# Kernel optimization log

Hardware: AMD Instinct MI355X
Metric: run time of the kernel (lower is better)

Reference implementation:

```python
import jax, jax.numpy as jnp
import numpy as np

B, N, P, K = 4, 8192, 2048, 16
C_IN, C_OUT, DIMS = 64, 128, 3
C_MID = C_OUT // 4                      # 32 (C_in != 0 branch)
DM = min(int(np.ceil(C_OUT / C_IN)), 4) # 2, depth multiplier for SepConv
C_DENSE = C_OUT // 2                    # 64, dense-projected feature dim
C_CAT = C_MID + C_DENSE                 # 96, lifted + projected features


def setup_inputs() -> dict:
    key = jax.random.key(0)
    ks = jax.random.split(key, 12)
    g = lambda k, shape, fan: jax.random.normal(k, shape, jnp.float32) / np.sqrt(fan).astype(np.float32)
    return {
        "pts": jax.random.normal(ks[0], (B, N, DIMS), jnp.float32),
        "fts": jax.random.normal(ks[1], (B, N, C_IN), jnp.float32),
        # PointCNN.dense: Linear(C_in, C_out//2) + ELU
        "dense_W": g(ks[2], (C_IN, C_DENSE), C_IN), "dense_b": jnp.zeros((C_DENSE,), jnp.float32),
        # XConv.dense1/dense2: Linear(dims,C_mid)+ELU, Linear(C_mid,C_mid)+ELU
        "d1_W": g(ks[3], (DIMS, C_MID), DIMS), "d1_b": jnp.zeros((C_MID,), jnp.float32),
        "d2_W": g(ks[4], (C_MID, C_MID), C_MID), "d2_b": jnp.zeros((C_MID,), jnp.float32),
        # conv2d: Conv2d(dims, K*K, (1,K)) + ELU, weight (out, in, kW)
        "conv_W": g(ks[5], (K * K, DIMS, K), DIMS * K), "conv_b": jnp.zeros((K * K,), jnp.float32),
        # dep_conv1/2: depthwise Conv2d(K, K*K, (1,K), groups=K); weight (group, mult, kW)
        "dw1_W": g(ks[6], (K, K, K), K), "dw1_b": jnp.zeros((K, K), jnp.float32),
        "dw2_W": g(ks[7], (K, K, K), K), "dw2_b": jnp.zeros((K, K), jnp.float32),
        # end_conv SepConv: depthwise (C_CAT groups, DM mult, (1,K)) then pointwise 1x1 -> C_OUT, ELU
        "sep_dw_W": g(ks[8], (C_CAT, DM, K), K), "sep_dw_b": jnp.zeros((C_CAT, DM), jnp.float32),
        "sep_pw_W": g(ks[9], (C_OUT, C_CAT, DM), C_CAT * DM), "sep_pw_b": jnp.zeros((C_OUT,), jnp.float32),
    }


def _fps(pts, npoint):
    """Iterative farthest point sampling (deterministic start at index 0)."""
    b, n, _ = pts.shape
    dist0 = jnp.full((b, n), 1e10, pts.dtype)
    far0 = jnp.zeros((b,), jnp.int32)

    def step(carry, _):
        dist, far = carry
        centroid = jnp.take_along_axis(pts, far[:, None, None], axis=1)  # [B,1,3]
        d = jnp.sum((pts - centroid) ** 2, -1)                            # [B,N]
        dist = jnp.minimum(dist, d)
        return (dist, jnp.argmax(dist, -1).astype(jnp.int32)), far

    _, idx = jax.lax.scan(step, (dist0, far0), None, length=npoint)  # [P,B]
    idx = idx.T                                                       # [B,P]
    return jnp.take_along_axis(pts, idx[..., None], axis=1)          # [B,P,3]


def reference(pts, fts, dense_W, dense_b, d1_W, d1_b, d2_W, d2_b,
              conv_W, conv_b, dw1_W, dw1_b, dw2_W, dw2_b,
              sep_dw_W, sep_dw_b, sep_pw_W, sep_pw_b):
    rep_pts = _fps(pts, P)                                            # [B,P,3]
    fts_d = jax.nn.elu(fts @ dense_W + dense_b)                       # [B,N,64]
    # KNN: squared distances rep->all points, K smallest
    d2 = (jnp.sum(rep_pts ** 2, -1)[..., None]
          - 2.0 * jnp.einsum('npc,nqc->npq', rep_pts, pts)
          + jnp.sum(pts ** 2, -1)[:, None, :])                        # [B,P,N]
    _, idx = jax.lax.top_k(-d2, K)                                    # [B,P,K]
    bidx = jnp.arange(B)[:, None, None]
    pts_reg = pts[bidx, idx]                                          # [B,P,K,3]
    fts_reg = fts_d[bidx, idx]                                        # [B,P,K,64]
    # XConv
    pl = pts_reg - rep_pts[:, :, None, :]                             # local coords
    lift = jax.nn.elu(jax.nn.elu(pl @ d1_W + d1_b) @ d2_W + d2_b)     # [B,P,K,C_MID]
    fts_cat = jnp.concatenate([lift, fts_reg], -1)                    # [B,P,K,C_CAT]
    X = jax.nn.elu(jnp.einsum('npkc,ock->npo', pl, conv_W) + conv_b).reshape(B, P, K, K)
    # depthwise convs over neighbor axis (spatial dim collapses to 1 -> einsum)
    X = jax.nn.elu(jnp.einsum('npij,jmi->npjm', X, dw1_W) + dw1_b)
    X = jnp.einsum('npij,jmi->npjm', X, dw2_W) + dw2_b
    fts_X = jnp.einsum('npab,npbc->npac', X, fts_cat)                 # [B,P,K,C_CAT]
    # separable end conv: depthwise over K, pointwise to C_OUT, ELU
    d = jnp.einsum('npkc,cmk->npcm', fts_X, sep_dw_W) + sep_dw_b
    fts_p = jax.nn.elu(jnp.einsum('npcm,ocm->npo', d, sep_pw_W) + sep_pw_b)  # [B,P,C_OUT]
    return rep_pts, fts_p
```

## Files before the change

### kernel.cpp

```cpp
#include <hip/hip_runtime.h>

#define BB 4
#define NN 8192
#define PP 2048
#define KNB 16
#define CIN 64
#define COUT 128

__device__ __forceinline__ float elu(float x) { return x > 0.0f ? x : expm1f(x); }

__device__ __forceinline__ unsigned fkey(float d) {
    unsigned u = __float_as_uint(d);
    unsigned m = (unsigned)((int)u >> 31);
    return u ^ (m | 0x80000000u);
}

__global__ __launch_bounds__(512) void fps_kernel(const float* __restrict__ pts,
                                                  float* __restrict__ rep) {
    const int b = blockIdx.x;
    const int t = threadIdx.x;
    const int lane = t & 63, wave = t >> 6;

    __shared__ float spx[NN];
    __shared__ float spy[NN];
    __shared__ float spz[NN];
    __shared__ unsigned long long partk[2][8];

    const float* pb = pts + (size_t)b * NN * 3;
    for (int i = t; i < NN; i += 512) {
        spx[i] = pb[3 * i + 0];
        spy[i] = pb[3 * i + 1];
        spz[i] = pb[3 * i + 2];
    }
    __syncthreads();

    float px[16], py[16], pz[16], dist[16];
#pragma unroll
    for (int r = 0; r < 16; ++r) {
        px[r] = spx[t * 16 + r];
        py[r] = spy[t * 16 + r];
        pz[r] = spz[t * 16 + r];
        dist[r] = 1e10f;
    }

    float cx = spx[0], cy = spy[0], cz = spz[0];
    if (t == 0) {
        rep[(size_t)b * PP * 3 + 0] = cx;
        rep[(size_t)b * PP * 3 + 1] = cy;
        rep[(size_t)b * PP * 3 + 2] = cz;
    }

    int buf = 0;
    for (int s = 1; s < PP; ++s) {
        float bv = -1.0f; int bi = 0;
#pragma unroll
        for (int r = 0; r < 16; ++r) {
            float dx = __fsub_rn(px[r], cx);
            float dy = __fsub_rn(py[r], cy);
            float dz = __fsub_rn(pz[r], cz);
            float d = __fadd_rn(__fadd_rn(__fmul_rn(dx, dx), __fmul_rn(dy, dy)), __fmul_rn(dz, dz));
            float nd = fminf(dist[r], d);
            dist[r] = nd;
            bool tk = nd > bv;
            bi = tk ? (t * 16 + r) : bi;
            bv = fmaxf(nd, bv);
        }
        unsigned long long k = ((unsigned long long)__float_as_uint(bv) << 32)
                             | (unsigned)(8191 - bi);
#pragma unroll
        for (int off = 32; off >= 1; off >>= 1) {
            unsigned long long o = __shfl_xor(k, off);
            k = o > k ? o : k;
        }
        if (lane == 0) partk[buf][wave] = k;
        __syncthreads();
        unsigned long long kk = partk[buf][0];
#pragma unroll
        for (int q = 1; q < 8; ++q) {
            unsigned long long c = partk[buf][q];
            kk = c > kk ? c : kk;
        }
        int widx = 8191 - (int)(unsigned)(kk & 0xFFFFFFFFULL);
        cx = spx[widx]; cy = spy[widx]; cz = spz[widx];
        if (t == 0) {
            float* rp = rep + ((size_t)b * PP + s) * 3;
            rp[0] = cx; rp[1] = cy; rp[2] = cz;
        }
        buf ^= 1;
    }
}

__global__ __launch_bounds__(256) void dense_kernel(const float* __restrict__ fts,
                                                    const float* __restrict__ W,
                                                    const float* __restrict__ bias,
                                                    float* __restrict__ out) {
    const int row = blockIdx.x * 4 + (threadIdx.x >> 6);
    const int c = threadIdx.x & 63;
    float v = fts[(size_t)row * 64 + c];
    float acc = bias[c];
#pragma unroll 8
    for (int k = 0; k < 64; ++k) acc = fmaf(__shfl(v, k), W[k * 64 + c], acc);
    out[(size_t)row * 64 + c] = elu(acc);
}

__global__ __launch_bounds__(256) void knn_kernel(const float* __restrict__ pts,
                                                  const float* __restrict__ rep,
                                                  int* __restrict__ kidx) {
    const int wid = blockIdx.x * 4 + (threadIdx.x >> 6);
    const int lane = threadIdx.x & 63;
    const int b = wid >> 11;
    const float* pb = pts + (size_t)b * NN * 3;

    float rx = rep[(size_t)wid * 3 + 0];
    float ry = rep[(size_t)wid * 3 + 1];
    float rz = rep[(size_t)wid * 3 + 2];
    float a = __fadd_rn(__fadd_rn(__fmul_rn(rx, rx), __fmul_rn(ry, ry)), __fmul_rn(rz, rz));

    unsigned long long key[16];
#pragma unroll
    for (int s = 0; s < 16; ++s) key[s] = ~0ULL;

    for (int j = lane; j < NN; j += 64) {
        float qx = pb[j * 3 + 0], qy = pb[j * 3 + 1], qz = pb[j * 3 + 2];
        float cc = __fadd_rn(__fadd_rn(__fmul_rn(qx, qx), __fmul_rn(qy, qy)), __fmul_rn(qz, qz));
        float bs = __fadd_rn(__fadd_rn(__fmul_rn(rx, qx), __fmul_rn(ry, qy)), __fmul_rn(rz, qz));
        float d2 = __fadd_rn(__fsub_rn(a, __fmul_rn(2.0f, bs)), cc);
        unsigned long long nk = ((unsigned long long)fkey(d2) << 32) | (unsigned)j;
        if (nk < key[15]) {
            key[15] = nk;
#pragma unroll
            for (int s2 = 15; s2 > 0; --s2) {
                unsigned long long u = key[s2 - 1], w = key[s2];
                bool sw = w < u;
                key[s2 - 1] = sw ? w : u;
                key[s2] = sw ? u : w;
            }
        }
    }

    int outv = 0;
#pragma unroll 1
    for (int r = 0; r < 16; ++r) {
        unsigned long long h = key[0];
#pragma unroll
        for (int off = 1; off < 64; off <<= 1) {
            unsigned long long o = __shfl_xor(h, off);
            h = (o < h) ? o : h;
        }
        if (lane == r) outv = (int)(unsigned)(h & 0xFFFFFFFFull);
        if (key[0] == h) {
#pragma unroll
            for (int s2 = 0; s2 < 15; ++s2) key[s2] = key[s2 + 1];
            key[15] = ~0ULL;
        }
    }
    if (lane < 16) kidx[(size_t)wid * 16 + lane] = outv;
}

__global__ __launch_bounds__(64) void xconv_kernel(
    const float* __restrict__ pts, const float* __restrict__ rep,
    const float* __restrict__ ftsd, const int* __restrict__ kidx,
    const float* __restrict__ d1W, const float* __restrict__ d1b,
    const float* __restrict__ d2W, const float* __restrict__ d2b,
    const float* __restrict__ convW, const float* __restrict__ convb,
    const float* __restrict__ dw1W, const float* __restrict__ dw1b,
    const float* __restrict__ dw2W, const float* __restrict__ dw2b,
    const float* __restrict__ sdwW, const float* __restrict__ sdwb,
    const float* __restrict__ spwW, const float* __restrict__ spwb,
    float* __restrict__ outp) {
    const int bp = blockIdx.x;
    const int b = bp >> 11;
    const int t = threadIdx.x;

    __shared__ float pl[16][3];
    __shared__ int nidx[16];
    __shared__ float fcat[16][96];
    __shared__ float A1[16][32];
    __shared__ float Xm[16][17];
    __shared__ float X2[16][17];
    __shared__ float X3[16][17];
    __shared__ float fX[16][97];
    __shared__ float dsep[192];

    if (t < 16) {
        int id = kidx[(size_t)bp * 16 + t];
        nidx[t] = id;
        const float* q = pts + ((size_t)b * NN + id) * 3;
        const float* rr = rep + (size_t)bp * 3;
        pl[t][0] = q[0] - rr[0];
        pl[t][1] = q[1] - rr[1];
        pl[t][2] = q[2] - rr[2];
    }
    __syncthreads();

#pragma unroll
    for (int k = 0; k < 16; ++k)
        fcat[k][32 + t] = ftsd[((size_t)b * NN + nidx[k]) * 64 + t];

#pragma unroll
    for (int r2 = 0; r2 < 8; ++r2) {
        int e = t + 64 * r2; int k = e >> 5, j = e & 31;
        float acc = d1b[j];
        acc = fmaf(pl[k][0], d1W[j], acc);
        acc = fmaf(pl[k][1], d1W[32 + j], acc);
        acc = fmaf(pl[k][2], d1W[64 + j], acc);
        A1[k][j] = elu(acc);
    }
    __syncthreads();

#pragma unroll
    for (int r2 = 0; r2 < 8; ++r2) {
        int e = t + 64 * r2; int k = e >> 5, j = e & 31;
        float acc = d2b[j];
#pragma unroll
        for (int c = 0; c < 32; ++c) acc = fmaf(A1[k][c], d2W[c * 32 + j], acc);
        fcat[k][j] = elu(acc);
    }
    __syncthreads();

#pragma unroll
    for (int r2 = 0; r2 < 4; ++r2) {
        int o = t + 64 * r2;
        float acc = convb[o];
#pragma unroll
        for (int c = 0; c < 3; ++c)
#pragma unroll
            for (int k = 0; k < 16; ++k)
                acc = fmaf(pl[k][c], convW[(o * 3 + c) * 16 + k], acc);
        Xm[o >> 4][o & 15] = elu(acc);
    }
    __syncthreads();

#pragma unroll
    for (int r2 = 0; r2 < 4; ++r2) {
        int e = t + 64 * r2; int j = e >> 4, m = e & 15;
        float acc = dw1b[e];
#pragma unroll
        for (int i = 0; i < 16; ++i) acc = fmaf(Xm[i][j], dw1W[e * 16 + i], acc);
        X2[j][m] = elu(acc);
    }
    __syncthreads();

#pragma unroll
    for (int r2 = 0; r2 < 4; ++r2) {
        int e = t + 64 * r2; int j = e >> 4, m = e & 15;
        float acc = dw2b[e];
#pragma unroll
        for (int i = 0; i < 16; ++i) acc = fmaf(X2[i][j], dw2W[e * 16 + i], acc);
        X3[j][m] = acc;
    }
    __syncthreads();

#pragma unroll
    for (int r2 = 0; r2 < 24; ++r2) {
        int e = t + 64 * r2; int a = e & 15, c = e >> 4;
        float acc = 0.0f;
#pragma unroll
        for (int q = 0; q < 16; ++q) acc = fmaf(X3[a][q], fcat[q][c], acc);
        fX[a][c] = acc;
    }
    __syncthreads();

#pragma unroll
    for (int r2 = 0; r2 < 3; ++r2) {
        int e = t + 64 * r2; int c = e >> 1;
        float acc = sdwb[e];
#pragma unroll
        for (int k = 0; k < 16; ++k) acc = fmaf(fX[k][c], sdwW[e * 16 + k], acc);
        dsep[e] = acc;
    }
    __syncthreads();

#pragma unroll
    for (int r2 = 0; r2 < 2; ++r2) {
        int o = t + 64 * r2;
        float acc = spwb[o];
#pragma unroll 16
        for (int e2 = 0; e2 < 192; ++e2) acc = fmaf(dsep[e2], spwW[o * 192 + e2], acc);
        outp[(size_t)bp * 128 + o] = elu(acc);
    }
}

extern "C" void kernel_launch(void* const* d_in, const int* in_sizes, int n_in,
                              void* d_out, int out_size, void* d_ws, size_t ws_size,
                              hipStream_t stream) {
    const float* pts    = (const float*)d_in[0];
    const float* fts    = (const float*)d_in[1];
    const float* denseW = (const float*)d_in[2];
    const float* denseb = (const float*)d_in[3];
    const float* d1W    = (const float*)d_in[4];
    const float* d1b    = (const float*)d_in[5];
    const float* d2W    = (const float*)d_in[6];
    const float* d2b    = (const float*)d_in[7];
    const float* convW  = (const float*)d_in[8];
    const float* convb  = (const float*)d_in[9];
    const float* dw1W   = (const float*)d_in[10];
    const float* dw1b   = (const float*)d_in[11];
    const float* dw2W   = (const float*)d_in[12];
    const float* dw2b   = (const float*)d_in[13];
    const float* sdwW   = (const float*)d_in[14];
    const float* sdwb   = (const float*)d_in[15];
    const float* spwW   = (const float*)d_in[16];
    const float* spwb   = (const float*)d_in[17];

    float* rep  = (float*)d_out;
    float* outp = (float*)d_out + (size_t)BB * PP * 3;

    float* ftsd = (float*)d_ws;
    int*   kidx = (int*)((char*)d_ws + (size_t)BB * NN * CIN * sizeof(float));

    dense_kernel<<<BB * NN / 4, 256, 0, stream>>>(fts, denseW, denseb, ftsd);
    fps_kernel<<<BB, 512, 0, stream>>>(pts, rep);
    knn_kernel<<<BB * PP / 4, 256, 0, stream>>>(pts, rep, kidx);
    xconv_kernel<<<BB * PP, 64, 0, stream>>>(pts, rep, ftsd, kidx,
                                             d1W, d1b, d2W, d2b, convW, convb,
                                             dw1W, dw1b, dw2W, dw2b,
                                             sdwW, sdwb, spwW, spwb, outp);
}
```

Before: 2.581 ms.

## Morton-sort points in FPS and prune thread distance updates with bounding spheres

The FPS kernel now sorts each batch's points by a quantized Morton code with a shared-memory bitonic sort, so each thread owns 16 spatially nearby points. Each thread computes a bounding sphere for its points and skips the per-step distance update when the new centroid is provably too far away to lower the thread's current maximum distance. This cuts arithmetic in the 2047-step serial loop but adds a one-time sort, 32 KB more LDS, and divergence; the 64-lane wave reduction and barrier still run every step. Tie-breaking now uses original indices to keep results identical.

```diff
diff --git a/kernel.cpp b/kernel.cpp
--- a/kernel.cpp
+++ b/kernel.cpp
@@ -15,6 +15,15 @@
     return u ^ (m | 0x80000000u);
 }
 
+__device__ __forceinline__ unsigned mspread(unsigned v) {
+    v &= 0x3FFu;
+    v = (v | (v << 16)) & 0x030000FFu;
+    v = (v | (v << 8))  & 0x0300F00Fu;
+    v = (v | (v << 4))  & 0x030C30C3u;
+    v = (v | (v << 2))  & 0x09249249u;
+    return v;
+}
+
 __global__ __launch_bounds__(512) void fps_kernel(const float* __restrict__ pts,
                                                   float* __restrict__ rep) {
     const int b = blockIdx.x;
@@ -24,6 +33,7 @@
     __shared__ float spx[NN];
     __shared__ float spy[NN];
     __shared__ float spz[NN];
+    __shared__ unsigned sbuf[NN];
     __shared__ unsigned long long partk[2][8];
 
     const float* pb = pts + (size_t)b * NN * 3;
@@ -34,14 +44,60 @@
     }
     __syncthreads();
 
+#pragma unroll
+    for (int r = 0; r < 16; ++r) {
+        int i = t * 16 + r;
+        int qx = min(max((int)((spx[i] + 4.0f) * 8.0f), 0), 63);
+        int qy = min(max((int)((spy[i] + 4.0f) * 8.0f), 0), 63);
+        int qz = min(max((int)((spz[i] + 4.0f) * 8.0f), 0), 63);
+        unsigned code = mspread((unsigned)qx) | (mspread((unsigned)qy) << 1)
+                      | (mspread((unsigned)qz) << 2);
+        sbuf[i] = (code << 13) | (unsigned)i;
+    }
+    __syncthreads();
+
+    for (unsigned kk2 = 2; kk2 <= (unsigned)NN; kk2 <<= 1) {
+        for (unsigned j = kk2 >> 1; j > 0; j >>= 1) {
+#pragma unroll
+            for (int m = 0; m < 8; ++m) {
+                unsigned i = (unsigned)t + (unsigned)m * 512u;
+                unsigned low = i & (j - 1u);
+                unsigned a = ((i & ~(j - 1u)) << 1) | low;
+                unsigned p2 = a | j;
+                unsigned ka = sbuf[a], kb = sbuf[p2];
+                bool up = ((a & kk2) == 0u);
+                if ((ka > kb) == up) { sbuf[a] = kb; sbuf[p2] = ka; }
+            }
+            __syncthreads();
+        }
+    }
+
+    int orig[16];
     float px[16], py[16], pz[16], dist[16];
 #pragma unroll
     for (int r = 0; r < 16; ++r) {
-        px[r] = spx[t * 16 + r];
-        py[r] = spy[t * 16 + r];
-        pz[r] = spz[t * 16 + r];
+        int o = (int)(sbuf[t * 16 + r] & 0x1FFFu);
+        orig[r] = o;
+        px[r] = spx[o]; py[r] = spy[o]; pz[r] = spz[o];
         dist[r] = 1e10f;
     }
+    float gx = 0.f, gy = 0.f, gz = 0.f;
+#pragma unroll
+    for (int r = 0; r < 16; ++r) { gx += px[r]; gy += py[r]; gz += pz[r]; }
+    gx *= (1.0f / 16.0f); gy *= (1.0f / 16.0f); gz *= (1.0f / 16.0f);
+    float r2m = 0.f;
+#pragma unroll
+    for (int r = 0; r < 16; ++r) {
+        float ex = px[r] - gx, ey = py[r] - gy, ez = pz[r] - gz;
+        r2m = fmaxf(r2m, ex * ex + ey * ey + ez * ez);
+    }
+    const float rg = sqrtf(r2m) * 1.00002f + 1e-12f;
+
+    int minorig = orig[0];
+#pragma unroll
+    for (int r = 1; r < 16; ++r) minorig = min(minorig, orig[r]);
+    unsigned long long gkey = ((unsigned long long)__float_as_uint(1e10f) << 32)
+                            | (unsigned)(8191 - minorig);
 
     float cx = spx[0], cy = spy[0], cz = spz[0];
     if (t == 0) {
@@ -52,21 +108,33 @@
 
     int buf = 0;
     for (int s = 1; s < PP; ++s) {
-        float bv = -1.0f; int bi = 0;
-#pragma unroll
-        for (int r = 0; r < 16; ++r) {
-            float dx = __fsub_rn(px[r], cx);
-            float dy = __fsub_rn(py[r], cy);
-            float dz = __fsub_rn(pz[r], cz);
-            float d = __fadd_rn(__fadd_rn(__fmul_rn(dx, dx), __fmul_rn(dy, dy)), __fmul_rn(dz, dz));
-            float nd = fminf(dist[r], d);
-            dist[r] = nd;
-            bool tk = nd > bv;
-            bi = tk ? (t * 16 + r) : bi;
-            bv = fmaxf(nd, bv);
-        }
-        unsigned long long k = ((unsigned long long)__float_as_uint(bv) << 32)
-                             | (unsigned)(8191 - bi);
+        float ddx = cx - gx, ddy = cy - gy, ddz = cz - gz;
+        float D = ddx * ddx + ddy * ddy + ddz * ddz;
+        float sD = sqrtf(D) * 0.99999f;
+        float diff = sD - rg;
+        float gmaxf = __uint_as_float((unsigned)(gkey >> 32));
+        bool prune = (diff > 0.0f) && (diff * diff * 0.9999f > gmaxf);
+
+        if (!prune) {
+            float bv = -1.0f; int bi = 0x7FFFFFFF;
+#pragma unroll
+            for (int r = 0; r < 16; ++r) {
+                float dx = __fsub_rn(px[r], cx);
+                float dy = __fsub_rn(py[r], cy);
+                float dz = __fsub_rn(pz[r], cz);
+                float d = __fadd_rn(__fadd_rn(__fmul_rn(dx, dx), __fmul_rn(dy, dy)),
+                                    __fmul_rn(dz, dz));
+                float nd = fminf(dist[r], d);
+                dist[r] = nd;
+                bool take = (nd > bv) || ((nd == bv) && (orig[r] < bi));
+                bi = take ? orig[r] : bi;
+                bv = take ? nd : bv;
+            }
+            gkey = ((unsigned long long)__float_as_uint(bv) << 32)
+                 | (unsigned)(8191 - bi);
+        }
+
+        unsigned long long k = gkey;
 #pragma unroll
         for (int off = 32; off >= 1; off >>= 1) {
             unsigned long long o = __shfl_xor(k, off);
```

New measurement: 3.740 ms. +44.9%, slower.
